# Performance work log

Measured on AMD Instinct MI355X. Metric: run time of the kernel, lower is better.

The kernel has to match this reference:

```python
import jax, jax.numpy as jnp
import numpy as np

BN_EPS = 1e-5


def setup_inputs() -> dict:
    key = jax.random.key(0)
    ks = jax.random.split(key, 4)
    B, N, D = 8, 8192, 256
    outD = 256
    s = 1.0 / np.sqrt(D)
    return {
        "feature": jax.random.normal(ks[0], (B, N, D), dtype=jnp.float32),
        "W_qk": jax.random.normal(ks[1], (2, D, D), dtype=jnp.float32) * s,
        "b_qk": jnp.zeros((2, D), dtype=jnp.float32),
        "W_v": jax.random.normal(ks[2], (D, outD), dtype=jnp.float32) * s,
        "b_v": jnp.zeros((outD,), dtype=jnp.float32),
        "gamma": jnp.ones((D,), dtype=jnp.float32),
        "beta": jnp.zeros((D,), dtype=jnp.float32),
    }


def reference(feature, W_qk, b_qk, W_v, b_v, gamma, beta):
    # QK: [B, 2, N, D]
    QK = jnp.einsum("bnd,kde->bkne", feature, W_qk) + b_qk[None, :, None, :]
    # value: [B, N, outD]
    value = jnp.einsum("bnd,de->bne", feature, W_v) + b_v
    query = QK[:, 0]  # [B, N, D]
    key = QK[:, 1]    # [B, N, D]
    # softmax over the sequence axis (dim=1), per (batch, channel)
    sm = jax.nn.softmax(key, axis=1)
    # lambda context: softmax^T @ value -> [B, D, outD]
    lam = jnp.einsum("bnd,bne->bde", sm, value)
    # BatchNorm1d(featureDim) in training mode: channel axis = D (axis 1),
    # stats over (batch, spatial) = axes (0, 2); biased variance as torch uses.
    mean = jnp.mean(lam, axis=(0, 2), keepdims=True)
    var = jnp.var(lam, axis=(0, 2), keepdims=True)
    bn = (lam - mean) * jax.lax.rsqrt(var + BN_EPS)
    bn = bn * gamma[None, :, None] + beta[None, :, None]
    # result: query @ BN -> [B, N, outD]
    return jnp.einsum("bnd,bde->bne", query, bn)
```

## Files before the change

### kernel.cpp

```cpp
#include <hip/hip_runtime.h>

typedef unsigned short u16;
typedef __bf16 bf16x8 __attribute__((ext_vector_type(8)));
typedef float f32x4 __attribute__((ext_vector_type(4)));

#define LOG2E 1.44269504088896f

__device__ inline u16 f2b(float f) {
    unsigned u = __float_as_uint(f);
    u += 0x7fff + ((u >> 16) & 1);
    return (u16)(u >> 16);
}
__device__ inline float b2f(u16 u) { return __uint_as_float(((unsigned)u) << 16); }
__device__ inline unsigned pk2(float a, float b) {
    return (unsigned)f2b(a) | ((unsigned)f2b(b) << 16);
}
__device__ inline uint4 pack8(float4 a, float4 b) {
    return uint4{pk2(a.x, a.y), pk2(a.z, a.w), pk2(b.x, b.y), pk2(b.z, b.w)};
}
__device__ inline f32x4 mfma_bf16(uint4 a, uint4 b, f32x4 c) {
    return __builtin_amdgcn_mfma_f32_16x16x32_bf16(
        __builtin_bit_cast(bf16x8, a), __builtin_bit_cast(bf16x8, b), c, 0, 0, 0);
}
__device__ inline void ld16(const u16* g, u16* l) {
    __builtin_amdgcn_global_load_lds(
        (const __attribute__((address_space(1))) unsigned int*)g,
        (__attribute__((address_space(3))) unsigned int*)l, 16, 0, 0);
}

__global__ __launch_bounds__(256) void prep_w(const float* __restrict__ Wqk,
                                              const float* __restrict__ Wv,
                                              u16* __restrict__ WkT,
                                              u16* __restrict__ WvT,
                                              u16* __restrict__ Wqb) {
    int idx = blockIdx.x * 256 + threadIdx.x;
    int which = idx >> 16;
    int i = (idx >> 8) & 255;
    int j = idx & 255;
    if (which == 0)
        WkT[i * 256 + j] = f2b(Wqk[65536 + j * 256 + i]);
    else if (which == 1)
        WvT[i * 256 + j] = f2b(Wv[j * 256 + i]);
    else
        Wqb[i * 256 + j] = f2b(Wqk[i * 256 + j]);
}

__global__ __launch_bounds__(256, 2) void gemm_kv(const float* __restrict__ A,
                                                  const u16* __restrict__ BtK,
                                                  const u16* __restrict__ BtV,
                                                  const float* __restrict__ biasK,
                                                  const float* __restrict__ biasV,
                                                  u16* __restrict__ KT,
                                                  u16* __restrict__ VT) {
    __shared__ __align__(16) u16 lds[18432];
    u16* As = lds;
    u16* BsK = lds + 2048;
    u16* BsV = lds + 10240;

    const int t = threadIdx.x;
    const int r0 = blockIdx.x * 64;
    const int w = t >> 6, lane = t & 63, l15 = lane & 15, q = lane >> 4;

    f32x4 accK[16], accV[16];
#pragma unroll
    for (int c = 0; c < 16; ++c) {
        accK[c] = f32x4{0.f, 0.f, 0.f, 0.f};
        accV[c] = f32x4{0.f, 0.f, 0.f, 0.f};
    }

    const int ar = t >> 2;
    const int ak = (t & 3) * 8;
    const float* Arow = A + (long)(r0 + ar) * 256 + ak;
    u16* AsW = As + t * 8;

    float4 a0 = ((const float4*)Arow)[0];
    float4 a1 = ((const float4*)Arow)[1];

    for (int k0 = 0; k0 < 256; k0 += 32) {
#pragma unroll
        for (int j = 0; j < 4; ++j) {
            int ch = j * 256 + t;
            int br = ch >> 2;
            int bk = (ch & 3) * 8;
            ld16(BtK + br * 256 + k0 + bk, BsK + j * 2048 + w * 512);
            ld16(BtV + br * 256 + k0 + bk, BsV + j * 2048 + w * 512);
        }
        *(uint4*)AsW = pack8(a0, a1);
        __syncthreads();
        if (k0 + 32 < 256) {
            a0 = ((const float4*)(Arow + k0 + 32))[0];
            a1 = ((const float4*)(Arow + k0 + 32))[1];
        }
        uint4 af = *(const uint4*)(As + (w * 16 + l15) * 32 + q * 8);
#pragma unroll
        for (int c = 0; c < 16; ++c) {
            uint4 bK = *(const uint4*)(BsK + (c * 16 + l15) * 32 + q * 8);
            uint4 bV = *(const uint4*)(BsV + (c * 16 + l15) * 32 + q * 8);
            accK[c] = mfma_bf16(af, bK, accK[c]);
            accV[c] = mfma_bf16(af, bV, accV[c]);
        }
        __syncthreads();
    }

    const int bb = r0 >> 13, n0 = r0 & 8191;
    u16* Ct = lds;
#pragma unroll
    for (int pass = 0; pass < 2; ++pass) {
        const f32x4* acc = pass ? accV : accK;
        const float* bias = pass ? biasV : biasK;
        u16* CT = pass ? VT : KT;
#pragma unroll
        for (int c = 0; c < 16; ++c) {
            float bv = bias[c * 16 + l15];
            ushort4 pk;
            pk.x = f2b(acc[c][0] + bv);
            pk.y = f2b(acc[c][1] + bv);
            pk.z = f2b(acc[c][2] + bv);
            pk.w = f2b(acc[c][3] + bv);
            *(ushort4*)&Ct[(c * 16 + l15) * 72 + w * 16 + q * 4] = pk;
        }
        __syncthreads();
        long off = ((long)bb * 256 + t) * 8192 + n0;
#pragma unroll
        for (int j = 0; j < 8; ++j)
            *(uint4*)(CT + off + j * 8) = *(const uint4*)&Ct[t * 72 + j * 8];
        __syncthreads();
    }
}

__global__ __launch_bounds__(256, 3) void gemm_out(const float* __restrict__ A,
                                                   const u16* __restrict__ WfoldT,
                                                   const float* __restrict__ outb,
                                                   float* __restrict__ C) {
    __shared__ __align__(16) u16 lds[10240];
    u16* As = lds;
    u16* Bs = lds + 2048;

    const int t = threadIdx.x;
    const int r0 = blockIdx.x * 64;
    const int bb = r0 >> 13;
    const int w = t >> 6, lane = t & 63, l15 = lane & 15, q = lane >> 4;
    const u16* Bt = WfoldT + (long)bb * 65536;

    f32x4 acc[16];
#pragma unroll
    for (int c = 0; c < 16; ++c) acc[c] = f32x4{0.f, 0.f, 0.f, 0.f};

    const float* Arow = A + (long)(r0 + (t >> 2)) * 256 + (t & 3) * 8;
    u16* AsW = As + t * 8;

    float4 a0 = ((const float4*)Arow)[0];
    float4 a1 = ((const float4*)Arow)[1];

    for (int k0 = 0; k0 < 256; k0 += 32) {
#pragma unroll
        for (int j = 0; j < 4; ++j) {
            int ch = j * 256 + t;
            ld16(Bt + (ch >> 2) * 256 + k0 + (ch & 3) * 8, Bs + j * 2048 + w * 512);
        }
        *(uint4*)AsW = pack8(a0, a1);
        __syncthreads();
        if (k0 + 32 < 256) {
            a0 = ((const float4*)(Arow + k0 + 32))[0];
            a1 = ((const float4*)(Arow + k0 + 32))[1];
        }
        uint4 af = *(const uint4*)(As + (w * 16 + l15) * 32 + q * 8);
#pragma unroll
        for (int c = 0; c < 16; ++c) {
            uint4 bf = *(const uint4*)(Bs + (c * 16 + l15) * 32 + q * 8);
            acc[c] = mfma_bf16(af, bf, acc[c]);
        }
        __syncthreads();
    }

#pragma unroll
    for (int c = 0; c < 16; ++c) {
        int col = c * 16 + l15;
        float bv = outb[bb * 256 + col];
#pragma unroll
        for (int r = 0; r < 4; ++r) {
            int row = r0 + w * 16 + q * 4 + r;
            C[(long)row * 256 + col] = acc[c][r] + bv;
        }
    }
}

__global__ __launch_bounds__(256, 4) void gemm_splitk(const u16* __restrict__ VT,
                                                      const u16* __restrict__ PT,
                                                      float* __restrict__ lamP,
                                                      int chunk) {
    __shared__ __align__(16) u16 lds[8192];
    u16* As = lds;
    u16* Bs = lds + 4096;

    const int t = threadIdx.x;
    const int r0 = blockIdx.x * 128;
    const int c0 = blockIdx.y * 128;
    const int s = blockIdx.z;
    const int bb = blockIdx.x >> 1;
    const long n0 = (long)s * chunk;
    const int w = t >> 6, lane = t & 63, l15 = lane & 15, q = lane >> 4;

    f32x4 acc[2][8];
#pragma unroll
    for (int rt = 0; rt < 2; ++rt)
#pragma unroll
        for (int c = 0; c < 8; ++c) acc[rt][c] = f32x4{0.f, 0.f, 0.f, 0.f};

    for (int k0 = 0; k0 < chunk; k0 += 32) {
#pragma unroll
        for (int j = 0; j < 2; ++j) {
            int ch = j * 256 + t;
            int br = ch >> 2;
            int bk = (ch & 3) * 8;
            ld16(VT + (long)(r0 + br) * 8192 + n0 + k0 + bk, As + j * 2048 + w * 512);
            ld16(PT + ((long)bb * 256 + c0 + br) * 8192 + n0 + k0 + bk,
                 Bs + j * 2048 + w * 512);
        }
        __syncthreads();
        uint4 af0 = *(const uint4*)(As + (w * 32 + l15) * 32 + q * 8);
        uint4 af1 = *(const uint4*)(As + (w * 32 + 16 + l15) * 32 + q * 8);
#pragma unroll
        for (int c = 0; c < 8; ++c) {
            uint4 bf = *(const uint4*)(Bs + (c * 16 + l15) * 32 + q * 8);
            acc[0][c] = mfma_bf16(af0, bf, acc[0][c]);
            acc[1][c] = mfma_bf16(af1, bf, acc[1][c]);
        }
        __syncthreads();
    }

    float* outp = lamP + (long)s * 524288;
#pragma unroll
    for (int rt = 0; rt < 2; ++rt)
#pragma unroll
        for (int c = 0; c < 8; ++c) {
            int col = c0 + c * 16 + l15;
#pragma unroll
            for (int r = 0; r < 4; ++r) {
                int row = r0 + w * 32 + rt * 16 + q * 4 + r;
                outp[(long)row * 256 + col] = acc[rt][c][r];
            }
        }
}

__global__ __launch_bounds__(256) void reduce_lam(const float* __restrict__ lamP,
                                                  float* __restrict__ lamT, int S) {
    int i = blockIdx.x * 256 + threadIdx.x;
    float4 v = ((const float4*)lamP)[i];
    for (int s = 1; s < S; ++s) {
        float4 p = ((const float4*)(lamP + (long)s * 524288))[i];
        v.x += p.x; v.y += p.y; v.z += p.z; v.w += p.w;
    }
    ((float4*)lamT)[i] = v;
}

__global__ __launch_bounds__(256, 4) void gemm_fold(const u16* __restrict__ Abn,
                                                    const u16* __restrict__ Wqb,
                                                    u16* __restrict__ WfoldT) {
    __shared__ __align__(16) u16 lds[4096];
    u16* As = lds;
    u16* Bs = lds + 2048;

    const int t = threadIdx.x;
    const int r0 = blockIdx.x * 64;
    const int c0 = blockIdx.y * 64;
    const int w = t >> 6, lane = t & 63, l15 = lane & 15, q = lane >> 4;

    f32x4 acc[4];
#pragma unroll
    for (int c = 0; c < 4; ++c) acc[c] = f32x4{0.f, 0.f, 0.f, 0.f};

    const int br = t >> 2;
    const int bk = (t & 3) * 8;

    for (int k0 = 0; k0 < 256; k0 += 32) {
        ld16(Abn + (long)(r0 + br) * 256 + k0 + bk, As + w * 512);
        ld16(Wqb + (long)(c0 + br) * 256 + k0 + bk, Bs + w * 512);
        __syncthreads();
        uint4 af = *(const uint4*)(As + (w * 16 + l15) * 32 + q * 8);
#pragma unroll
        for (int c = 0; c < 4; ++c) {
            uint4 bf = *(const uint4*)(Bs + (c * 16 + l15) * 32 + q * 8);
            acc[c] = mfma_bf16(af, bf, acc[c]);
        }
        __syncthreads();
    }

#pragma unroll
    for (int c = 0; c < 4; ++c) {
        int col = c0 + c * 16 + l15;
#pragma unroll
        for (int r = 0; r < 4; ++r) {
            int row = r0 + w * 16 + q * 4 + r;
            WfoldT[(long)row * 256 + col] = f2b(acc[c][r]);
        }
    }
}

__global__ __launch_bounds__(64) void softmax_rows(u16* __restrict__ KT) {
    const int row = blockIdx.x;
    const int lane = threadIdx.x;
    u16* p = KT + (long)row * 8192;

    uint4 buf[16];
#pragma unroll
    for (int i = 0; i < 16; ++i) buf[i] = *(const uint4*)(p + (i * 64 + lane) * 8);

    float m = -1e30f;
#pragma unroll
    for (int i = 0; i < 16; ++i) {
        const unsigned* u = (const unsigned*)&buf[i];
#pragma unroll
        for (int j = 0; j < 4; ++j) {
            m = fmaxf(m, fmaxf(b2f((u16)(u[j] & 0xffff)), b2f((u16)(u[j] >> 16))));
        }
    }
#pragma unroll
    for (int s = 32; s > 0; s >>= 1) m = fmaxf(m, __shfl_xor(m, s, 64));

    float sum = 0.f;
#pragma unroll
    for (int i = 0; i < 16; ++i) {
        const unsigned* u = (const unsigned*)&buf[i];
#pragma unroll
        for (int j = 0; j < 4; ++j) {
            sum += exp2f((b2f((u16)(u[j] & 0xffff)) - m) * LOG2E);
            sum += exp2f((b2f((u16)(u[j] >> 16)) - m) * LOG2E);
        }
    }
#pragma unroll
    for (int s = 32; s > 0; s >>= 1) sum += __shfl_xor(sum, s, 64);
    float rl = 1.0f / sum;

#pragma unroll
    for (int i = 0; i < 16; ++i) {
        unsigned* u = (unsigned*)&buf[i];
#pragma unroll
        for (int j = 0; j < 4; ++j) {
            float a = exp2f((b2f((u16)(u[j] & 0xffff)) - m) * LOG2E) * rl;
            float b = exp2f((b2f((u16)(u[j] >> 16)) - m) * LOG2E) * rl;
            u[j] = (unsigned)f2b(a) | ((unsigned)f2b(b) << 16);
        }
        *(uint4*)(p + (i * 64 + lane) * 8) = buf[i];
    }
}

__global__ __launch_bounds__(256) void bn_kernel(const float* __restrict__ lamT,
                                                 const float* __restrict__ gamma,
                                                 const float* __restrict__ beta,
                                                 u16* __restrict__ bnT) {
    const int d = blockIdx.x;
    const int t = threadIdx.x;
    float vals[8];
    float s = 0.f, ss = 0.f;
#pragma unroll
    for (int i = 0; i < 8; ++i) {
        float v = lamT[(long)(i * 256 + t) * 256 + d];
        vals[i] = v;
        s += v;
        ss += v * v;
    }
#pragma unroll
    for (int sh = 32; sh > 0; sh >>= 1) {
        s += __shfl_xor(s, sh, 64);
        ss += __shfl_xor(ss, sh, 64);
    }
    __shared__ float red[8];
    int w = t >> 6;
    if ((t & 63) == 0) {
        red[w] = s;
        red[w + 4] = ss;
    }
    __syncthreads();
    s = red[0] + red[1] + red[2] + red[3];
    ss = red[4] + red[5] + red[6] + red[7];
    float mean = s * (1.f / 2048.f);
    float var = ss * (1.f / 2048.f) - mean * mean;
    float scale = gamma[d] * rsqrtf(var + 1e-5f);
    float shift = beta[d] - mean * scale;
#pragma unroll
    for (int i = 0; i < 8; ++i)
        bnT[(long)(i * 256 + t) * 256 + d] = f2b(vals[i] * scale + shift);
}

__global__ __launch_bounds__(256) void outb_kernel(const float* __restrict__ bq,
                                                   const u16* __restrict__ bnT,
                                                   float* __restrict__ outb) {
    int b = blockIdx.x, e = threadIdx.x;
    const u16* rowp = bnT + ((long)b * 256 + e) * 256;
    float s = 0.f;
    for (int dd = 0; dd < 256; ++dd) s += bq[dd] * b2f(rowp[dd]);
    outb[b * 256 + e] = s;
}

extern "C" void kernel_launch(void* const* d_in, const int* in_sizes, int n_in,
                              void* d_out, int out_size, void* d_ws, size_t ws_size,
                              hipStream_t stream) {
    const float* feat = (const float*)d_in[0];
    const float* W_qk = (const float*)d_in[1];
    const float* b_qk = (const float*)d_in[2];
    const float* W_v = (const float*)d_in[3];
    const float* b_v = (const float*)d_in[4];
    const float* gamma = (const float*)d_in[5];
    const float* beta = (const float*)d_in[6];
    float* out = (float*)d_out;

    char* ws = (char*)d_ws;
    u16* KT = (u16*)(ws);
    u16* VT = (u16*)(ws + 33554432);
    u16* WkT = (u16*)(ws + 67108864);
    u16* WvT = (u16*)(ws + 67239936);
    u16* Wqb = (u16*)(ws + 67371008);
    const size_t base = 67502080;
    float* lamP = (float*)(ws + base);
    size_t avail = (ws_size > base) ? ws_size - base : 0;
    int S = (avail >= 16u * 2097152u) ? 16
          : (avail >= 8u * 2097152u) ? 8
          : (avail >= 4u * 2097152u) ? 4 : 2;
    float* lamT = (float*)ws;
    u16* bnT = (u16*)(ws + 2097152);
    u16* WfoldT = (u16*)(ws + 3145728);
    float* outb = (float*)(ws + 4194304);

    prep_w<<<768, 256, 0, stream>>>(W_qk, W_v, WkT, WvT, Wqb);
    gemm_kv<<<1024, 256, 0, stream>>>(feat, WkT, WvT, b_qk + 256, b_v, KT, VT);
    softmax_rows<<<2048, 64, 0, stream>>>(KT);
    gemm_splitk<<<dim3(16, 2, S), 256, 0, stream>>>(VT, KT, lamP, 8192 / S);
    reduce_lam<<<512, 256, 0, stream>>>(lamP, lamT, S);
    bn_kernel<<<256, 256, 0, stream>>>(lamT, gamma, beta, bnT);
    outb_kernel<<<8, 256, 0, stream>>>(b_qk, bnT, outb);
    gemm_fold<<<dim3(32, 4), 256, 0, stream>>>(bnT, Wqb, WfoldT);
    gemm_out<<<1024, 256, 0, stream>>>(feat, WfoldT, outb, out);
}
```

Measured before the change: 253.2 us.

## Use 32x32 MFMA with 128-row tiles and register double buffering in projection GEMMs

The fused K/V projection kernel becomes a generic 128-row-tile GEMM launched once for K and once for V. Both it and the output GEMM now use 32x32x16 bf16 MFMA, with double-buffered LDS filled from register prefetch instead of global_load_lds. The split-K partials go into the output buffer as scratch with a fixed split of 16, removing the workspace-size logic. The larger tiles raise data reuse per block and overlap global loads with compute, but splitting K and V means the fp32 feature input is read twice.

Measured after the change: 262.2 us. 3.5% more time.

```diff
diff --git a/kernel.cpp b/kernel.cpp
--- a/kernel.cpp
+++ b/kernel.cpp
@@ -3,6 +3,7 @@
 typedef unsigned short u16;
 typedef __bf16 bf16x8 __attribute__((ext_vector_type(8)));
 typedef float f32x4 __attribute__((ext_vector_type(4)));
+typedef float f32x16 __attribute__((ext_vector_type(16)));
 
 #define LOG2E 1.44269504088896f
 
@@ -18,8 +19,12 @@
 __device__ inline uint4 pack8(float4 a, float4 b) {
     return uint4{pk2(a.x, a.y), pk2(a.z, a.w), pk2(b.x, b.y), pk2(b.z, b.w)};
 }
-__device__ inline f32x4 mfma_bf16(uint4 a, uint4 b, f32x4 c) {
+__device__ inline f32x4 mfma16(uint4 a, uint4 b, f32x4 c) {
     return __builtin_amdgcn_mfma_f32_16x16x32_bf16(
+        __builtin_bit_cast(bf16x8, a), __builtin_bit_cast(bf16x8, b), c, 0, 0, 0);
+}
+__device__ inline f32x16 mfma32(uint4 a, uint4 b, f32x16 c) {
+    return __builtin_amdgcn_mfma_f32_32x32x16_bf16(
         __builtin_bit_cast(bf16x8, a), __builtin_bit_cast(bf16x8, b), c, 0, 0, 0);
 }
 __device__ inline void ld16(const u16* g, u16* l) {
@@ -45,142 +50,154 @@
         Wqb[i * 256 + j] = f2b(Wqk[i * 256 + j]);
 }
 
-__global__ __launch_bounds__(256, 2) void gemm_kv(const float* __restrict__ A,
-                                                  const u16* __restrict__ BtK,
-                                                  const u16* __restrict__ BtV,
-                                                  const float* __restrict__ biasK,
-                                                  const float* __restrict__ biasV,
-                                                  u16* __restrict__ KT,
-                                                  u16* __restrict__ VT) {
-    __shared__ __align__(16) u16 lds[18432];
+
+#define G32_LOADG(k0)                                                     \
+    {                                                                     \
+        ga0 = ((const float4*)(Arow + (k0)))[0];                          \
+        ga1 = ((const float4*)(Arow + (k0)))[1];                          \
+        ga2 = ((const float4*)(Arow + (k0)))[2];                          \
+        ga3 = ((const float4*)(Arow + (k0)))[3];                          \
+        gb0 = *(const uint4*)(Brow + (k0));                               \
+        gb1 = *(const uint4*)(Brow + (k0) + 8);                           \
+        gb2 = *(const uint4*)(Brow + (k0) + 16);                          \
+        gb3 = *(const uint4*)(Brow + (k0) + 24);                          \
+    }
+#define G32_STORE(p)                                                      \
+    {                                                                     \
+        *(uint4*)(AsW + (p)*4096) = pack8(ga0, ga1);                      \
+        *(uint4*)(AsW + (p)*4096 + 1024) = pack8(ga2, ga3);               \
+        *(uint4*)(BsW + (p)*8192) = gb0;                                  \
+        *(uint4*)(BsW + (p)*8192 + 2048) = gb1;                           \
+        *(uint4*)(BsW + (p)*8192 + 4096) = gb2;                           \
+        *(uint4*)(BsW + (p)*8192 + 6144) = gb3;                           \
+    }
+
+__global__ __launch_bounds__(256, 2) void gemm_proj(const float* __restrict__ A,
+                                                    const u16* __restrict__ Bt,
+                                                    const float* __restrict__ bias,
+                                                    u16* __restrict__ CT) {
+    __shared__ __align__(16) u16 lds[24576];
     u16* As = lds;
-    u16* BsK = lds + 2048;
-    u16* BsV = lds + 10240;
+    u16* Bs = lds + 8192;
 
     const int t = threadIdx.x;
-    const int r0 = blockIdx.x * 64;
-    const int w = t >> 6, lane = t & 63, l15 = lane & 15, q = lane >> 4;
-
-    f32x4 accK[16], accV[16];
-#pragma unroll
-    for (int c = 0; c < 16; ++c) {
-        accK[c] = f32x4{0.f, 0.f, 0.f, 0.f};
-        accV[c] = f32x4{0.f, 0.f, 0.f, 0.f};
-    }
-
-    const int ar = t >> 2;
-    const int ak = (t & 3) * 8;
-    const float* Arow = A + (long)(r0 + ar) * 256 + ak;
-    u16* AsW = As + t * 8;
-
-    float4 a0 = ((const float4*)Arow)[0];
-    float4 a1 = ((const float4*)Arow)[1];
-
+    const int r0 = blockIdx.x * 128;
+    const int w = t >> 6, lane = t & 63, l31 = lane & 31, h = lane >> 5;
+
+    f32x16 acc[8];
+#pragma unroll
+    for (int c = 0; c < 8; ++c) acc[c] = (f32x16)0.f;
+
+    const int tr = t >> 1, ts = t & 1;
+    const float* Arow = A + (long)(r0 + tr) * 256 + ts * 16;
+    const u16* Brow = Bt + t * 256;
+    u16* AsW = As + ts * 2048 + tr * 8;
+    u16* BsW = Bs + t * 8;
+    const u16* AsR = As + h * 1024 + (w * 32 + l31) * 8;
+    const u16* BsR = Bs + h * 2048 + l31 * 8;
+
+    float4 ga0, ga1, ga2, ga3;
+    uint4 gb0, gb1, gb2, gb3;
+
+    G32_LOADG(0);
+    G32_STORE(0);
+    __syncthreads();
     for (int k0 = 0; k0 < 256; k0 += 32) {
-#pragma unroll
-        for (int j = 0; j < 4; ++j) {
-            int ch = j * 256 + t;
-            int br = ch >> 2;
-            int bk = (ch & 3) * 8;
-            ld16(BtK + br * 256 + k0 + bk, BsK + j * 2048 + w * 512);
-            ld16(BtV + br * 256 + k0 + bk, BsV + j * 2048 + w * 512);
-        }
-        *(uint4*)AsW = pack8(a0, a1);
-        __syncthreads();
-        if (k0 + 32 < 256) {
-            a0 = ((const float4*)(Arow + k0 + 32))[0];
-            a1 = ((const float4*)(Arow + k0 + 32))[1];
-        }
-        uint4 af = *(const uint4*)(As + (w * 16 + l15) * 32 + q * 8);
-#pragma unroll
-        for (int c = 0; c < 16; ++c) {
-            uint4 bK = *(const uint4*)(BsK + (c * 16 + l15) * 32 + q * 8);
-            uint4 bV = *(const uint4*)(BsV + (c * 16 + l15) * 32 + q * 8);
-            accK[c] = mfma_bf16(af, bK, accK[c]);
-            accV[c] = mfma_bf16(af, bV, accV[c]);
-        }
+        const int p = (k0 >> 5) & 1;
+        if (k0 + 32 < 256) G32_LOADG(k0 + 32);
+#pragma unroll
+        for (int s = 0; s < 2; ++s) {
+            uint4 af = *(const uint4*)(AsR + p * 4096 + s * 2048);
+#pragma unroll
+            for (int ct = 0; ct < 8; ++ct) {
+                uint4 bf = *(const uint4*)(BsR + p * 8192 + s * 4096 + ct * 256);
+                acc[ct] = mfma32(af, bf, acc[ct]);
+            }
+        }
+        if (k0 + 32 < 256) G32_STORE(p ^ 1);
         __syncthreads();
     }
 
     const int bb = r0 >> 13, n0 = r0 & 8191;
     u16* Ct = lds;
 #pragma unroll
-    for (int pass = 0; pass < 2; ++pass) {
-        const f32x4* acc = pass ? accV : accK;
-        const float* bias = pass ? biasV : biasK;
-        u16* CT = pass ? VT : KT;
-#pragma unroll
-        for (int c = 0; c < 16; ++c) {
-            float bv = bias[c * 16 + l15];
-            ushort4 pk;
-            pk.x = f2b(acc[c][0] + bv);
-            pk.y = f2b(acc[c][1] + bv);
-            pk.z = f2b(acc[c][2] + bv);
-            pk.w = f2b(acc[c][3] + bv);
-            *(ushort4*)&Ct[(c * 16 + l15) * 72 + w * 16 + q * 4] = pk;
-        }
-        __syncthreads();
-        long off = ((long)bb * 256 + t) * 8192 + n0;
+    for (int half = 0; half < 2; ++half) {
+        __syncthreads();
+#pragma unroll
+        for (int c4 = 0; c4 < 4; ++c4) {
+            const int ct = half * 4 + c4;
+            const int dl = c4 * 32 + l31;
+            const float bv = bias[half * 128 + dl];
+#pragma unroll
+            for (int r = 0; r < 16; ++r) {
+                int nl = w * 32 + (r & 3) + 8 * (r >> 2) + 4 * h;
+                Ct[dl * 136 + nl] = f2b(acc[ct][r] + bv);
+            }
+        }
+        __syncthreads();
+        long off = ((long)bb * 256 + half * 128 + (t >> 1)) * 8192 + n0 + (t & 1) * 64;
+        const u16* src = Ct + (t >> 1) * 136 + (t & 1) * 64;
 #pragma unroll
         for (int j = 0; j < 8; ++j)
-            *(uint4*)(CT + off + j * 8) = *(const uint4*)&Ct[t * 72 + j * 8];
-        __syncthreads();
-    }
-}
-
-__global__ __launch_bounds__(256, 3) void gemm_out(const float* __restrict__ A,
+            *(uint4*)(CT + off + j * 8) = *(const uint4*)(src + j * 8);
+    }
+}
+
+__global__ __launch_bounds__(256, 2) void gemm_out(const float* __restrict__ A,
                                                    const u16* __restrict__ WfoldT,
                                                    const float* __restrict__ outb,
                                                    float* __restrict__ C) {
-    __shared__ __align__(16) u16 lds[10240];
+    __shared__ __align__(16) u16 lds[24576];
     u16* As = lds;
-    u16* Bs = lds + 2048;
+    u16* Bs = lds + 8192;
 
     const int t = threadIdx.x;
-    const int r0 = blockIdx.x * 64;
+    const int r0 = blockIdx.x * 128;
     const int bb = r0 >> 13;
-    const int w = t >> 6, lane = t & 63, l15 = lane & 15, q = lane >> 4;
-    const u16* Bt = WfoldT + (long)bb * 65536;
-
-    f32x4 acc[16];
-#pragma unroll
-    for (int c = 0; c < 16; ++c) acc[c] = f32x4{0.f, 0.f, 0.f, 0.f};
-
-    const float* Arow = A + (long)(r0 + (t >> 2)) * 256 + (t & 3) * 8;
-    u16* AsW = As + t * 8;
-
-    float4 a0 = ((const float4*)Arow)[0];
-    float4 a1 = ((const float4*)Arow)[1];
-
+    const int w = t >> 6, lane = t & 63, l31 = lane & 31, h = lane >> 5;
+
+    f32x16 acc[8];
+#pragma unroll
+    for (int c = 0; c < 8; ++c) acc[c] = (f32x16)0.f;
+
+    const int tr = t >> 1, ts = t & 1;
+    const float* Arow = A + (long)(r0 + tr) * 256 + ts * 16;
+    const u16* Brow = WfoldT + (long)bb * 65536 + t * 256;
+    u16* AsW = As + ts * 2048 + tr * 8;
+    u16* BsW = Bs + t * 8;
+    const u16* AsR = As + h * 1024 + (w * 32 + l31) * 8;
+    const u16* BsR = Bs + h * 2048 + l31 * 8;
+
+    float4 ga0, ga1, ga2, ga3;
+    uint4 gb0, gb1, gb2, gb3;
+
+    G32_LOADG(0);
+    G32_STORE(0);
+    __syncthreads();
     for (int k0 = 0; k0 < 256; k0 += 32) {
-#pragma unroll
-        for (int j = 0; j < 4; ++j) {
-            int ch = j * 256 + t;
-            ld16(Bt + (ch >> 2) * 256 + k0 + (ch & 3) * 8, Bs + j * 2048 + w * 512);
-        }
-        *(uint4*)AsW = pack8(a0, a1);
-        __syncthreads();
-        if (k0 + 32 < 256) {
-            a0 = ((const float4*)(Arow + k0 + 32))[0];
-            a1 = ((const float4*)(Arow + k0 + 32))[1];
-        }
-        uint4 af = *(const uint4*)(As + (w * 16 + l15) * 32 + q * 8);
-#pragma unroll
-        for (int c = 0; c < 16; ++c) {
-            uint4 bf = *(const uint4*)(Bs + (c * 16 + l15) * 32 + q * 8);
-            acc[c] = mfma_bf16(af, bf, acc[c]);
-        }
-        __syncthreads();
-    }
-
-#pragma unroll
-    for (int c = 0; c < 16; ++c) {
-        int col = c * 16 + l15;
-        float bv = outb[bb * 256 + col];
-#pragma unroll
-        for (int r = 0; r < 4; ++r) {
-            int row = r0 + w * 16 + q * 4 + r;
-            C[(long)row * 256 + col] = acc[c][r] + bv;
+        const int p = (k0 >> 5) & 1;
+        if (k0 + 32 < 256) G32_LOADG(k0 + 32);
+#pragma unroll
+        for (int s = 0; s < 2; ++s) {
+            uint4 af = *(const uint4*)(AsR + p * 4096 + s * 2048);
+#pragma unroll
+            for (int ct = 0; ct < 8; ++ct) {
+                uint4 bf = *(const uint4*)(BsR + p * 8192 + s * 4096 + ct * 256);
+                acc[ct] = mfma32(af, bf, acc[ct]);
+            }
+        }
+        if (k0 + 32 < 256) G32_STORE(p ^ 1);
+        __syncthreads();
+    }
+
+#pragma unroll
+    for (int ct = 0; ct < 8; ++ct) {
+        const int col = ct * 32 + l31;
+        const float bv = outb[bb * 256 + col];
+#pragma unroll
+        for (int r = 0; r < 16; ++r) {
+            int row = r0 + w * 32 + (r & 3) + 8 * (r >> 2) + 4 * h;
+            C[(long)row * 256 + col] = acc[ct][r] + bv;
         }
     }
 }
@@ -223,8 +240,8 @@
 #pragma unroll
         for (int c = 0; c < 8; ++c) {
             uint4 bf = *(const uint4*)(Bs + (c * 16 + l15) * 32 + q * 8);
-            acc[0][c] = mfma_bf16(af0, bf, acc[0][c]);
-            acc[1][c] = mfma_bf16(af1, bf, acc[1][c]);
+            acc[0][c] = mfma16(af0, bf, acc[0][c]);
+            acc[1][c] = mfma16(af1, bf, acc[1][c]);
         }
         __syncthreads();
     }
@@ -281,7 +298,7 @@
 #pragma unroll
         for (int c = 0; c < 4; ++c) {
             uint4 bf = *(const uint4*)(Bs + (c * 16 + l15) * 32 + q * 8);
-            acc[c] = mfma_bf16(af, bf, acc[c]);
+            acc[c] = mfma16(af, bf, acc[c]);
         }
         __syncthreads();
     }
@@ -411,24 +428,20 @@
     u16* WkT = (u16*)(ws + 67108864);
     u16* WvT = (u16*)(ws + 67239936);
     u16* Wqb = (u16*)(ws + 67371008);
-    const size_t base = 67502080;
-    float* lamP = (float*)(ws + base);
-    size_t avail = (ws_size > base) ? ws_size - base : 0;
-    int S = (avail >= 16u * 2097152u) ? 16
-          : (avail >= 8u * 2097152u) ? 8
-          : (avail >= 4u * 2097152u) ? 4 : 2;
-    float* lamT = (float*)ws;
-    u16* bnT = (u16*)(ws + 2097152);
-    u16* WfoldT = (u16*)(ws + 3145728);
+    float* lamT = (float*)(ws + 67502080);
+    float* lamPd = (float*)d_out;
+    u16* bnT = (u16*)ws;
+    u16* WfoldT = (u16*)(ws + 2097152);
     float* outb = (float*)(ws + 4194304);
 
     prep_w<<<768, 256, 0, stream>>>(W_qk, W_v, WkT, WvT, Wqb);
-    gemm_kv<<<1024, 256, 0, stream>>>(feat, WkT, WvT, b_qk + 256, b_v, KT, VT);
+    gemm_proj<<<512, 256, 0, stream>>>(feat, WkT, b_qk + 256, KT);
+    gemm_proj<<<512, 256, 0, stream>>>(feat, WvT, b_v, VT);
     softmax_rows<<<2048, 64, 0, stream>>>(KT);
-    gemm_splitk<<<dim3(16, 2, S), 256, 0, stream>>>(VT, KT, lamP, 8192 / S);
-    reduce_lam<<<512, 256, 0, stream>>>(lamP, lamT, S);
+    gemm_splitk<<<dim3(16, 2, 16), 256, 0, stream>>>(VT, KT, lamPd, 512);
+    reduce_lam<<<512, 256, 0, stream>>>(lamPd, lamT, 16);
     bn_kernel<<<256, 256, 0, stream>>>(lamT, gamma, beta, bnT);
     outb_kernel<<<8, 256, 0, stream>>>(b_qk, bnT, outb);
     gemm_fold<<<dim3(32, 4), 256, 0, stream>>>(bnT, Wqb, WfoldT);
-    gemm_out<<<1024, 256, 0, stream>>>(feat, WfoldT, outb, out);
-}
+    gemm_out<<<512, 256, 0, stream>>>(feat, WfoldT, outb, out);
+}
```

## Switch GEMMs to 32x32x16 MFMA, cache bf16 features, use output as split-K scratch

Applied to the files above, without the earlier changes.

Rewrites gemm_kv, gemm_out and gemm_splitk to use the 32x32x16 bf16 MFMA with new k-split LDS layouts, in place of the 16x16x32 instruction. gemm_kv also writes a bf16 copy of the input features to workspace when space allows, so gemm_out can load them with direct global-to-LDS loads instead of reading and converting fp32 again. Split-K partials now go into the output buffer with a fixed 16-way split, which removes the dependence on workspace size. The costs are an extra 32 MB bf16 write in the first GEMM and changed occupancy hints (gemm_out goes from 3 to 2 blocks, splitk from 4 to 2).

Measured after the change: 296.2 us. +17.0%, slower.

```diff
diff --git a/kernel.cpp b/kernel.cpp
--- a/kernel.cpp
+++ b/kernel.cpp
@@ -3,6 +3,7 @@
 typedef unsigned short u16;
 typedef __bf16 bf16x8 __attribute__((ext_vector_type(8)));
 typedef float f32x4 __attribute__((ext_vector_type(4)));
+typedef float f32x16 __attribute__((ext_vector_type(16)));
 
 #define LOG2E 1.44269504088896f
 
@@ -18,8 +19,12 @@
 __device__ inline uint4 pack8(float4 a, float4 b) {
     return uint4{pk2(a.x, a.y), pk2(a.z, a.w), pk2(b.x, b.y), pk2(b.z, b.w)};
 }
-__device__ inline f32x4 mfma_bf16(uint4 a, uint4 b, f32x4 c) {
+__device__ inline f32x4 mfma16(uint4 a, uint4 b, f32x4 c) {
     return __builtin_amdgcn_mfma_f32_16x16x32_bf16(
+        __builtin_bit_cast(bf16x8, a), __builtin_bit_cast(bf16x8, b), c, 0, 0, 0);
+}
+__device__ inline f32x16 mfma32(uint4 a, uint4 b, f32x16 c) {
+    return __builtin_amdgcn_mfma_f32_32x32x16_bf16(
         __builtin_bit_cast(bf16x8, a), __builtin_bit_cast(bf16x8, b), c, 0, 0, 0);
 }
 __device__ inline void ld16(const u16* g, u16* l) {
@@ -45,59 +50,62 @@
         Wqb[i * 256 + j] = f2b(Wqk[i * 256 + j]);
 }
 
-__global__ __launch_bounds__(256, 2) void gemm_kv(const float* __restrict__ A,
-                                                  const u16* __restrict__ BtK,
-                                                  const u16* __restrict__ BtV,
-                                                  const float* __restrict__ biasK,
-                                                  const float* __restrict__ biasV,
-                                                  u16* __restrict__ KT,
-                                                  u16* __restrict__ VT) {
+__global__ __launch_bounds__(256, 2) void gemm_kvx(const float* __restrict__ A,
+                                                   const u16* __restrict__ BtK,
+                                                   const u16* __restrict__ BtV,
+                                                   const float* __restrict__ biasK,
+                                                   const float* __restrict__ biasV,
+                                                   u16* __restrict__ KT,
+                                                   u16* __restrict__ VT,
+                                                   u16* __restrict__ Xb) {
     __shared__ __align__(16) u16 lds[18432];
     u16* As = lds;
-    u16* BsK = lds + 2048;
-    u16* BsV = lds + 10240;
+    u16* Bs = lds + 2048;
 
     const int t = threadIdx.x;
     const int r0 = blockIdx.x * 64;
-    const int w = t >> 6, lane = t & 63, l15 = lane & 15, q = lane >> 4;
-
-    f32x4 accK[16], accV[16];
-#pragma unroll
-    for (int c = 0; c < 16; ++c) {
-        accK[c] = f32x4{0.f, 0.f, 0.f, 0.f};
-        accV[c] = f32x4{0.f, 0.f, 0.f, 0.f};
-    }
-
-    const int ar = t >> 2;
-    const int ak = (t & 3) * 8;
-    const float* Arow = A + (long)(r0 + ar) * 256 + ak;
-    u16* AsW = As + t * 8;
+    const int w = t >> 6, lane = t & 63, l31 = lane & 31, h = lane >> 5;
+    const int rh = w & 1, chalf = w >> 1;
+
+    f32x16 acc[8];
+#pragma unroll
+    for (int c = 0; c < 8; ++c) acc[c] = (f32x16)0.f;
+
+    const int ar = t >> 2, asg = t & 3;
+    const float* Arow = A + (long)(r0 + ar) * 256 + asg * 8;
+    u16* AsW = As + (asg >> 1) * 1024 + (asg & 1) * 512 + ar * 8;
+    u16* XbW = Xb ? Xb + (long)(r0 + ar) * 256 + asg * 8 : (u16*)0;
 
     float4 a0 = ((const float4*)Arow)[0];
     float4 a1 = ((const float4*)Arow)[1];
 
     for (int k0 = 0; k0 < 256; k0 += 32) {
 #pragma unroll
-        for (int j = 0; j < 4; ++j) {
-            int ch = j * 256 + t;
-            int br = ch >> 2;
-            int bk = (ch & 3) * 8;
-            ld16(BtK + br * 256 + k0 + bk, BsK + j * 2048 + w * 512);
-            ld16(BtV + br * 256 + k0 + bk, BsV + j * 2048 + w * 512);
-        }
-        *(uint4*)AsW = pack8(a0, a1);
-        __syncthreads();
+        for (int j = 0; j < 8; ++j) {
+            const int s = j >> 2, hh = (j >> 1) & 1, rb = j & 1;
+            const u16* src = rb ? BtV : BtK;
+            ld16(src + t * 256 + k0 + s * 16 + hh * 8,
+                 Bs + s * 8192 + hh * 4096 + rb * 2048 + w * 512);
+        }
+        uint4 ap = pack8(a0, a1);
+        *(uint4*)AsW = ap;
+        if (XbW) *(uint4*)(XbW + k0) = ap;
         if (k0 + 32 < 256) {
             a0 = ((const float4*)(Arow + k0 + 32))[0];
             a1 = ((const float4*)(Arow + k0 + 32))[1];
         }
-        uint4 af = *(const uint4*)(As + (w * 16 + l15) * 32 + q * 8);
-#pragma unroll
-        for (int c = 0; c < 16; ++c) {
-            uint4 bK = *(const uint4*)(BsK + (c * 16 + l15) * 32 + q * 8);
-            uint4 bV = *(const uint4*)(BsV + (c * 16 + l15) * 32 + q * 8);
-            accK[c] = mfma_bf16(af, bK, accK[c]);
-            accV[c] = mfma_bf16(af, bV, accV[c]);
+        __syncthreads();
+#pragma unroll
+        for (int s = 0; s < 2; ++s) {
+            uint4 af = *(const uint4*)(As + s * 1024 + h * 512 + (rh * 32 + l31) * 8);
+#pragma unroll
+            for (int pass = 0; pass < 2; ++pass)
+#pragma unroll
+                for (int ctl = 0; ctl < 4; ++ctl) {
+                    uint4 bf = *(const uint4*)(Bs + s * 8192 + h * 4096 +
+                                               (pass * 256 + chalf * 128 + ctl * 32 + l31) * 8);
+                    acc[pass * 4 + ctl] = mfma32(af, bf, acc[pass * 4 + ctl]);
+                }
         }
         __syncthreads();
     }
@@ -106,32 +114,37 @@
     u16* Ct = lds;
 #pragma unroll
     for (int pass = 0; pass < 2; ++pass) {
-        const f32x4* acc = pass ? accV : accK;
         const float* bias = pass ? biasV : biasK;
         u16* CT = pass ? VT : KT;
-#pragma unroll
-        for (int c = 0; c < 16; ++c) {
-            float bv = bias[c * 16 + l15];
-            ushort4 pk;
-            pk.x = f2b(acc[c][0] + bv);
-            pk.y = f2b(acc[c][1] + bv);
-            pk.z = f2b(acc[c][2] + bv);
-            pk.w = f2b(acc[c][3] + bv);
-            *(ushort4*)&Ct[(c * 16 + l15) * 72 + w * 16 + q * 4] = pk;
+        __syncthreads();
+#pragma unroll
+        for (int ctl = 0; ctl < 4; ++ctl) {
+            const int d = chalf * 128 + ctl * 32 + l31;
+            const float bv = bias[d];
+            const f32x16 a = acc[pass * 4 + ctl];
+#pragma unroll
+            for (int rg = 0; rg < 4; ++rg) {
+                ushort4 pk4;
+                pk4.x = f2b(a[rg * 4 + 0] + bv);
+                pk4.y = f2b(a[rg * 4 + 1] + bv);
+                pk4.z = f2b(a[rg * 4 + 2] + bv);
+                pk4.w = f2b(a[rg * 4 + 3] + bv);
+                *(ushort4*)&Ct[d * 68 + rh * 32 + rg * 8 + h * 4] = pk4;
+            }
         }
         __syncthreads();
         long off = ((long)bb * 256 + t) * 8192 + n0;
 #pragma unroll
         for (int j = 0; j < 8; ++j)
-            *(uint4*)(CT + off + j * 8) = *(const uint4*)&Ct[t * 72 + j * 8];
-        __syncthreads();
-    }
-}
-
-__global__ __launch_bounds__(256, 3) void gemm_out(const float* __restrict__ A,
-                                                   const u16* __restrict__ WfoldT,
-                                                   const float* __restrict__ outb,
-                                                   float* __restrict__ C) {
+            *(uint4*)(CT + off + j * 8) = *(const uint4*)&Ct[t * 68 + j * 8];
+    }
+}
+
+__global__ __launch_bounds__(256, 2) void gemm_out32(const float* __restrict__ Af,
+                                                     const u16* __restrict__ Xb,
+                                                     const u16* __restrict__ WfoldT,
+                                                     const float* __restrict__ outb,
+                                                     float* __restrict__ C) {
     __shared__ __align__(16) u16 lds[10240];
     u16* As = lds;
     u16* Bs = lds + 2048;
@@ -139,108 +152,125 @@
     const int t = threadIdx.x;
     const int r0 = blockIdx.x * 64;
     const int bb = r0 >> 13;
-    const int w = t >> 6, lane = t & 63, l15 = lane & 15, q = lane >> 4;
+    const int w = t >> 6, lane = t & 63, l31 = lane & 31, h = lane >> 5;
+    const int rh = w & 1, chalf = w >> 1;
     const u16* Bt = WfoldT + (long)bb * 65536;
 
-    f32x4 acc[16];
-#pragma unroll
-    for (int c = 0; c < 16; ++c) acc[c] = f32x4{0.f, 0.f, 0.f, 0.f};
-
-    const float* Arow = A + (long)(r0 + (t >> 2)) * 256 + (t & 3) * 8;
-    u16* AsW = As + t * 8;
-
-    float4 a0 = ((const float4*)Arow)[0];
-    float4 a1 = ((const float4*)Arow)[1];
+    f32x16 acc[4];
+#pragma unroll
+    for (int c = 0; c < 4; ++c) acc[c] = (f32x16)0.f;
+
+    const int ar = t >> 2, asg = t & 3;
+    const float* Arow = Af + (long)(r0 + ar) * 256 + asg * 8;
+    u16* AsW = As + (asg >> 1) * 1024 + (asg & 1) * 512 + ar * 8;
+    const u16* XbR = Xb ? Xb + (long)(r0 + lane) * 256 + w * 8 : (u16*)0;
+
+    float4 a0, a1;
+    if (!Xb) {
+        a0 = ((const float4*)Arow)[0];
+        a1 = ((const float4*)Arow)[1];
+    }
 
     for (int k0 = 0; k0 < 256; k0 += 32) {
 #pragma unroll
         for (int j = 0; j < 4; ++j) {
-            int ch = j * 256 + t;
-            ld16(Bt + (ch >> 2) * 256 + k0 + (ch & 3) * 8, Bs + j * 2048 + w * 512);
-        }
-        *(uint4*)AsW = pack8(a0, a1);
-        __syncthreads();
-        if (k0 + 32 < 256) {
-            a0 = ((const float4*)(Arow + k0 + 32))[0];
-            a1 = ((const float4*)(Arow + k0 + 32))[1];
-        }
-        uint4 af = *(const uint4*)(As + (w * 16 + l15) * 32 + q * 8);
-#pragma unroll
-        for (int c = 0; c < 16; ++c) {
-            uint4 bf = *(const uint4*)(Bs + (c * 16 + l15) * 32 + q * 8);
-            acc[c] = mfma_bf16(af, bf, acc[c]);
-        }
-        __syncthreads();
-    }
-
-#pragma unroll
-    for (int c = 0; c < 16; ++c) {
-        int col = c * 16 + l15;
-        float bv = outb[bb * 256 + col];
-#pragma unroll
-        for (int r = 0; r < 4; ++r) {
-            int row = r0 + w * 16 + q * 4 + r;
-            C[(long)row * 256 + col] = acc[c][r] + bv;
-        }
-    }
-}
-
-__global__ __launch_bounds__(256, 4) void gemm_splitk(const u16* __restrict__ VT,
-                                                      const u16* __restrict__ PT,
-                                                      float* __restrict__ lamP,
-                                                      int chunk) {
-    __shared__ __align__(16) u16 lds[8192];
+            const int s = j >> 1, hh = j & 1;
+            ld16(Bt + t * 256 + k0 + s * 16 + hh * 8, Bs + s * 4096 + hh * 2048 + w * 512);
+        }
+        if (Xb) {
+            ld16(XbR + k0, As + w * 512);
+        } else {
+            *(uint4*)AsW = pack8(a0, a1);
+            if (k0 + 32 < 256) {
+                a0 = ((const float4*)(Arow + k0 + 32))[0];
+                a1 = ((const float4*)(Arow + k0 + 32))[1];
+            }
+        }
+        __syncthreads();
+#pragma unroll
+        for (int s = 0; s < 2; ++s) {
+            uint4 af = *(const uint4*)(As + s * 1024 + h * 512 + (rh * 32 + l31) * 8);
+#pragma unroll
+            for (int ctl = 0; ctl < 4; ++ctl) {
+                uint4 bf = *(const uint4*)(Bs + s * 4096 + h * 2048 +
+                                           (chalf * 128 + ctl * 32 + l31) * 8);
+                acc[ctl] = mfma32(af, bf, acc[ctl]);
+            }
+        }
+        __syncthreads();
+    }
+
+#pragma unroll
+    for (int ctl = 0; ctl < 4; ++ctl) {
+        const int col = chalf * 128 + ctl * 32 + l31;
+        const float bv = outb[bb * 256 + col];
+#pragma unroll
+        for (int rg = 0; rg < 4; ++rg)
+#pragma unroll
+            for (int i = 0; i < 4; ++i) {
+                int row = r0 + rh * 32 + rg * 8 + h * 4 + i;
+                C[(long)row * 256 + col] = acc[ctl][rg * 4 + i] + bv;
+            }
+    }
+}
+
+__global__ __launch_bounds__(256, 2) void gemm_splitk32(const u16* __restrict__ VT,
+                                                        const u16* __restrict__ PT,
+                                                        float* __restrict__ lamP,
+                                                        int chunk) {
+    __shared__ __align__(16) u16 lds[16384];
     u16* As = lds;
-    u16* Bs = lds + 4096;
+    u16* Bs = lds + 8192;
 
     const int t = threadIdx.x;
     const int r0 = blockIdx.x * 128;
     const int c0 = blockIdx.y * 128;
-    const int s = blockIdx.z;
-    const int bb = blockIdx.x >> 1;
-    const long n0 = (long)s * chunk;
-    const int w = t >> 6, lane = t & 63, l15 = lane & 15, q = lane >> 4;
-
-    f32x4 acc[2][8];
-#pragma unroll
-    for (int rt = 0; rt < 2; ++rt)
-#pragma unroll
-        for (int c = 0; c < 8; ++c) acc[rt][c] = f32x4{0.f, 0.f, 0.f, 0.f};
+    const int z = blockIdx.z;
+    const int bb = r0 >> 8;
+    const long n0 = (long)z * chunk;
+    const int w = t >> 6, lane = t & 63, l31 = lane & 31, h = lane >> 5;
+    const int ws2 = w >> 1, wh = w & 1;
+
+    f32x16 acc[4];
+#pragma unroll
+    for (int c = 0; c < 4; ++c) acc[c] = (f32x16)0.f;
+
+    const u16* Asrc = VT + (long)r0 * 8192 + n0 + ws2 * 16 + wh * 8;
+    const u16* Bsrc = PT + ((long)bb * 256 + c0) * 8192 + n0 + ws2 * 16 + wh * 8;
 
     for (int k0 = 0; k0 < chunk; k0 += 32) {
 #pragma unroll
         for (int j = 0; j < 2; ++j) {
-            int ch = j * 256 + t;
-            int br = ch >> 2;
-            int bk = (ch & 3) * 8;
-            ld16(VT + (long)(r0 + br) * 8192 + n0 + k0 + bk, As + j * 2048 + w * 512);
-            ld16(PT + ((long)bb * 256 + c0 + br) * 8192 + n0 + k0 + bk,
-                 Bs + j * 2048 + w * 512);
-        }
-        __syncthreads();
-        uint4 af0 = *(const uint4*)(As + (w * 32 + l15) * 32 + q * 8);
-        uint4 af1 = *(const uint4*)(As + (w * 32 + 16 + l15) * 32 + q * 8);
-#pragma unroll
-        for (int c = 0; c < 8; ++c) {
-            uint4 bf = *(const uint4*)(Bs + (c * 16 + l15) * 32 + q * 8);
-            acc[0][c] = mfma_bf16(af0, bf, acc[0][c]);
-            acc[1][c] = mfma_bf16(af1, bf, acc[1][c]);
-        }
-        __syncthreads();
-    }
-
-    float* outp = lamP + (long)s * 524288;
-#pragma unroll
-    for (int rt = 0; rt < 2; ++rt)
-#pragma unroll
-        for (int c = 0; c < 8; ++c) {
-            int col = c0 + c * 16 + l15;
-#pragma unroll
-            for (int r = 0; r < 4; ++r) {
-                int row = r0 + w * 32 + rt * 16 + q * 4 + r;
-                outp[(long)row * 256 + col] = acc[rt][c][r];
-            }
-        }
+            ld16(Asrc + (long)(j * 64 + lane) * 8192 + k0,
+                 As + ws2 * 2048 + wh * 1024 + j * 512);
+            ld16(Bsrc + (long)(j * 64 + lane) * 8192 + k0,
+                 Bs + ws2 * 2048 + wh * 1024 + j * 512);
+        }
+        __syncthreads();
+#pragma unroll
+        for (int s = 0; s < 2; ++s) {
+            uint4 af = *(const uint4*)(As + s * 2048 + h * 1024 + (w * 32 + l31) * 8);
+#pragma unroll
+            for (int ct = 0; ct < 4; ++ct) {
+                uint4 bf = *(const uint4*)(Bs + s * 2048 + h * 1024 + (ct * 32 + l31) * 8);
+                acc[ct] = mfma32(af, bf, acc[ct]);
+            }
+        }
+        __syncthreads();
+    }
+
+    float* outp = lamP + (long)z * 524288;
+#pragma unroll
+    for (int ct = 0; ct < 4; ++ct) {
+        const int col = c0 + ct * 32 + l31;
+#pragma unroll
+        for (int rg = 0; rg < 4; ++rg)
+#pragma unroll
+            for (int i = 0; i < 4; ++i) {
+                int row = r0 + w * 32 + rg * 8 + h * 4 + i;
+                outp[(long)row * 256 + col] = acc[ct][rg * 4 + i];
+            }
+    }
 }
 
 __global__ __launch_bounds__(256) void reduce_lam(const float* __restrict__ lamP,
@@ -281,7 +311,7 @@
 #pragma unroll
         for (int c = 0; c < 4; ++c) {
             uint4 bf = *(const uint4*)(Bs + (c * 16 + l15) * 32 + q * 8);
-            acc[c] = mfma_bf16(af, bf, acc[c]);
+            acc[c] = mfma16(af, bf, acc[c]);
         }
         __syncthreads();
     }
@@ -411,24 +441,20 @@
     u16* WkT = (u16*)(ws + 67108864);
     u16* WvT = (u16*)(ws + 67239936);
     u16* Wqb = (u16*)(ws + 67371008);
-    const size_t base = 67502080;
-    float* lamP = (float*)(ws + base);
-    size_t avail = (ws_size > base) ? ws_size - base : 0;
-    int S = (avail >= 16u * 2097152u) ? 16
-          : (avail >= 8u * 2097152u) ? 8
-          : (avail >= 4u * 2097152u) ? 4 : 2;
-    float* lamT = (float*)ws;
-    u16* bnT = (u16*)(ws + 2097152);
-    u16* WfoldT = (u16*)(ws + 3145728);
+    float* lamT = (float*)(ws + 67502080);
+    u16* Xb = (ws_size >= 103153664u) ? (u16*)(ws + 69599232) : (u16*)0;
+    float* lamPd = (float*)d_out;
+    u16* bnT = (u16*)ws;
+    u16* WfoldT = (u16*)(ws + 2097152);
     float* outb = (float*)(ws + 4194304);
 
     prep_w<<<768, 256, 0, stream>>>(W_qk, W_v, WkT, WvT, Wqb);
-    gemm_kv<<<1024, 256, 0, stream>>>(feat, WkT, WvT, b_qk + 256, b_v, KT, VT);
+    gemm_kvx<<<1024, 256, 0, stream>>>(feat, WkT, WvT, b_qk + 256, b_v, KT, VT, Xb);
     softmax_rows<<<2048, 64, 0, stream>>>(KT);
-    gemm_splitk<<<dim3(16, 2, S), 256, 0, stream>>>(VT, KT, lamP, 8192 / S);
-    reduce_lam<<<512, 256, 0, stream>>>(lamP, lamT, S);
+    gemm_splitk32<<<dim3(16, 2, 16), 256, 0, stream>>>(VT, KT, lamPd, 512);
+    reduce_lam<<<512, 256, 0, stream>>>(lamPd, lamT, 16);
     bn_kernel<<<256, 256, 0, stream>>>(lamT, gamma, beta, bnT);
     outb_kernel<<<8, 256, 0, stream>>>(b_qk, bnT, outb);
     gemm_fold<<<dim3(32, 4), 256, 0, stream>>>(bnT, Wqb, WfoldT);
-    gemm_out<<<1024, 256, 0, stream>>>(feat, WfoldT, outb, out);
-}
+    gemm_out32<<<1024, 256, 0, stream>>>(feat, Xb, WfoldT, outb, out);
+}
```
